# Performance work log

Measured on AMD Instinct MI355X. Metric: run time of the kernel, lower is better.

## Reference

```python
import jax, jax.numpy as jnp
import numpy as np

HIDDEN = 512
BATCH = 32
SEQ = 4096


def setup_inputs() -> dict:
    key = jax.random.key(0)
    ks = jax.random.split(key, 8)
    s = 1.0 / np.sqrt(HIDDEN)
    return {
        "encoder_outputs": jax.random.normal(ks[0], (BATCH, SEQ, HIDDEN), jnp.float32),
        "decoder_hidden": jax.random.normal(ks[1], (BATCH, HIDDEN), jnp.float32),
        "W_enc": jax.random.uniform(ks[2], (HIDDEN, HIDDEN), jnp.float32, -s, s),
        "b_enc": jax.random.uniform(ks[3], (HIDDEN,), jnp.float32, -s, s),
        "W_dec": jax.random.uniform(ks[4], (HIDDEN, HIDDEN), jnp.float32, -s, s),
        "b_dec": jax.random.uniform(ks[5], (HIDDEN,), jnp.float32, -s, s),
        "W_v": jax.random.uniform(ks[6], (HIDDEN, 1), jnp.float32, -s, s),
        "b_v": jax.random.uniform(ks[7], (1,), jnp.float32, -s, s),
    }


def reference(encoder_outputs, decoder_hidden, W_enc, b_enc, W_dec, b_dec, W_v, b_v):
    # (b, s, h) projected encoder states
    enc_proj = jnp.einsum("bsh,hk->bsk", encoder_outputs, W_enc) + b_enc
    # (b, 1, h) projected decoder state, broadcast-added over seq
    dec_proj = (decoder_hidden @ W_dec + b_dec)[:, None, :]
    # score: (b, s, 1)
    score = jnp.tanh(enc_proj + dec_proj) @ W_v + b_v
    attention_weights = jax.nn.softmax(score, axis=1)  # softmax over seq_len
    # context: (b, h) weighted sum of encoder outputs
    context = jnp.sum(attention_weights * encoder_outputs, axis=1)
    return context, jnp.squeeze(attention_weights, -1)
```

## Files before the change

### kernel.cpp

```cpp
#include <hip/hip_runtime.h>
#include <hip/hip_bf16.h>

typedef __attribute__((ext_vector_type(8))) short bf16x8;
typedef __attribute__((ext_vector_type(4))) float f32x4;

#define HID 512
#define NB 32
#define SEQL 4096
#define BM 64
#define NBLK 2048

#define WS_BP    0
#define WS_DPROJ (512*1024)
#define WS_SUM   (576*1024)

__device__ __forceinline__ short f2bf(float f) {
    unsigned u = __float_as_uint(f);
    unsigned r = (u + 0x7fffu + ((u >> 16) & 1u)) >> 16;
    return (short)r;
}

__device__ __forceinline__ float fast_tanh(float x) {
    float e = __expf(2.0f * x);
    float r = __builtin_amdgcn_rcpf(e + 1.0f);
    return 1.0f - 2.0f * r;
}

__device__ __forceinline__ void async16(const void* g, void* l) {
    __builtin_amdgcn_global_load_lds((__attribute__((address_space(1))) void*)(g),
                                     (__attribute__((address_space(3))) void*)(l),
                                     16, 0, 0);
}

__global__ void k_pre(const float* __restrict__ We, short* __restrict__ Bp,
                      const float* __restrict__ dec, const float* __restrict__ Wd,
                      const float* __restrict__ be, const float* __restrict__ bd,
                      float* __restrict__ dproj, float* __restrict__ out,
                      float* __restrict__ sumacc) {
    const int blk = blockIdx.x, t = threadIdx.x;
    if (blk < 128) {
        int tid  = blk * 256 + t;
        int lane = tid & 63;
        int nt   = (tid >> 6) & 31;
        int kc   = tid >> 11;
        int k0   = kc * 32 + (lane >> 4) * 8;
        int n    = nt * 16 + (lane & 15);
        bf16x8 v;
#pragma unroll
        for (int j = 0; j < 8; ++j) v[j] = f2bf(We[(size_t)(k0 + j) * HID + n]);
        *(bf16x8*)&Bp[(size_t)tid * 8] = v;
    } else if (blk < 640) {
        __shared__ float red[8][33];
        int bid2 = blk - 128;
        int b  = bid2 >> 4, kg = bid2 & 15;
        int kl = t & 31,    hc = t >> 5;
        int k  = kg * 32 + kl;
        const float* dr = dec + (size_t)b * HID;
        float a = 0.f;
#pragma unroll 8
        for (int j = 0; j < 64; ++j) {
            int h = hc * 64 + j;
            a += dr[h] * Wd[(size_t)h * HID + k];
        }
        red[hc][kl] = a;
        __syncthreads();
        if (hc == 0) {
            float s = be[k] + bd[k];
#pragma unroll
            for (int c = 0; c < 8; ++c) s += red[c][kl];
            dproj[(size_t)b * HID + k] = s;
        }
    } else {
        int bz = blk - 640;
        out[bz * 256 + t] = 0.f;
        if (bz == 0 && t < NB) sumacc[t] = 0.f;
    }
}

__global__ __launch_bounds__(256, 2)
void k_main(const float* __restrict__ E, const short* __restrict__ Bp,
            const float* __restrict__ dproj, const float* __restrict__ Wv,
            float* __restrict__ out, float* __restrict__ sumacc) {
    __shared__ short As[2][BM][40];
    __shared__ short Bs[2][32 * HID];
    __shared__ float fbuf[640];
    __shared__ float pbuf[BM];

    const int tid  = threadIdx.x;
    const int wave = tid >> 6, lane = tid & 63;
    const int quad = lane >> 4, l15 = lane & 15;
    const int bid  = blockIdx.x;
    const int row0 = bid * BM;
    const int b    = bid >> 6;

    f32x4 acc[4][8];
#pragma unroll
    for (int r = 0; r < 4; ++r)
#pragma unroll
        for (int c = 0; c < 8; ++c) acc[r][c] = (f32x4){0.f, 0.f, 0.f, 0.f};

    const int arow = tid >> 2, ac8 = (tid & 3) * 8;
    const float* aptr = E + (size_t)(row0 + arow) * HID + ac8;

    {
        float4 a0 = *(const float4*)(aptr);
        float4 a1 = *(const float4*)(aptr + 4);
#pragma unroll
        for (int i = 0; i < 8; ++i) {
            int off = (i * 4 + wave) * 512;
            async16(Bp + off + lane * 8, &Bs[0][off]);
        }
        bf16x8 av;
        av[0] = f2bf(a0.x); av[1] = f2bf(a0.y); av[2] = f2bf(a0.z); av[3] = f2bf(a0.w);
        av[4] = f2bf(a1.x); av[5] = f2bf(a1.y); av[6] = f2bf(a1.z); av[7] = f2bf(a1.w);
        *(bf16x8*)&As[0][arow][ac8] = av;
        __syncthreads();
    }

    for (int kc = 0; kc < 16; ++kc) {
        const int cur = kc & 1, nxt = cur ^ 1;
        float4 a0, a1;
        if (kc < 15) {
            a0 = *(const float4*)(aptr + (kc + 1) * 32);
            a1 = *(const float4*)(aptr + (kc + 1) * 32 + 4);
            const short* bsrc = Bp + (size_t)(kc + 1) * 16384;
#pragma unroll
            for (int i = 0; i < 8; ++i) {
                int off = (i * 4 + wave) * 512;
                async16(bsrc + off + lane * 8, &Bs[nxt][off]);
            }
        }
        bf16x8 fa[4];
#pragma unroll
        for (int r = 0; r < 4; ++r)
            fa[r] = *(bf16x8*)&As[cur][r * 16 + l15][quad * 8];
#pragma unroll
        for (int c = 0; c < 8; ++c) {
            int nt = wave * 8 + c;
            bf16x8 fb = *(bf16x8*)&Bs[cur][(nt * 64 + lane) * 8];
#pragma unroll
            for (int r = 0; r < 4; ++r)
                acc[r][c] = __builtin_amdgcn_mfma_f32_16x16x32_bf16(fa[r], fb, acc[r][c], 0, 0, 0);
        }
        if (kc < 15) {
            bf16x8 av;
            av[0] = f2bf(a0.x); av[1] = f2bf(a0.y); av[2] = f2bf(a0.z); av[3] = f2bf(a0.w);
            av[4] = f2bf(a1.x); av[5] = f2bf(a1.y); av[6] = f2bf(a1.z); av[7] = f2bf(a1.w);
            *(bf16x8*)&As[nxt][arow][ac8] = av;
        }
        __syncthreads();
    }

    float part[4][4];
#pragma unroll
    for (int r = 0; r < 4; ++r)
#pragma unroll
        for (int g = 0; g < 4; ++g) part[r][g] = 0.f;
    const float* dp = dproj + (size_t)b * HID;
#pragma unroll
    for (int c = 0; c < 8; ++c) {
        int col = wave * 128 + c * 16 + l15;
        float dv = dp[col];
        float wv = Wv[col];
#pragma unroll
        for (int r = 0; r < 4; ++r)
#pragma unroll
            for (int g = 0; g < 4; ++g)
                part[r][g] += fast_tanh(acc[r][c][g] + dv) * wv;
    }
#pragma unroll
    for (int r = 0; r < 4; ++r)
#pragma unroll
        for (int g = 0; g < 4; ++g) {
            float v = part[r][g];
            v += __shfl_xor(v, 1); v += __shfl_xor(v, 2);
            v += __shfl_xor(v, 4); v += __shfl_xor(v, 8);
            part[r][g] = v;
        }
    if (l15 == 0) {
#pragma unroll
        for (int r = 0; r < 4; ++r)
#pragma unroll
            for (int g = 0; g < 4; ++g)
                fbuf[wave * 64 + r * 16 + quad * 4 + g] = part[r][g];
    }
    __syncthreads();
    if (tid < 64) {
        float s  = fbuf[tid] + fbuf[64 + tid] + fbuf[128 + tid] + fbuf[192 + tid];
        float pv = __expf(s);
        pbuf[tid] = pv;
        out[(size_t)NB * HID + row0 + tid] = pv;
        float t2 = pv;
        t2 += __shfl_xor(t2, 1);  t2 += __shfl_xor(t2, 2);  t2 += __shfl_xor(t2, 4);
        t2 += __shfl_xor(t2, 8);  t2 += __shfl_xor(t2, 16); t2 += __shfl_xor(t2, 32);
        if (tid == 0) atomicAdd(&sumacc[b], t2);
    }
    __syncthreads();

    const int hq = tid & 127, rh = tid >> 7;
    const float4* E4 = (const float4*)E;
    size_t cbase = (size_t)(row0 + rh * 32) * (HID / 4) + hq;
    float4 ca = {0.f, 0.f, 0.f, 0.f};
#pragma unroll 4
    for (int rr = 0; rr < 32; ++rr) {
        float w  = pbuf[rh * 32 + rr];
        float4 e = E4[cbase + (size_t)rr * (HID / 4)];
        ca.x += w * e.x; ca.y += w * e.y; ca.z += w * e.z; ca.w += w * e.w;
    }
    if (rh == 1) {
        fbuf[hq] = ca.x; fbuf[128 + hq] = ca.y; fbuf[256 + hq] = ca.z; fbuf[384 + hq] = ca.w;
    }
    __syncthreads();
    if (rh == 0) {
        ca.x += fbuf[hq]; ca.y += fbuf[128 + hq]; ca.z += fbuf[256 + hq]; ca.w += fbuf[384 + hq];
        float* cg = out + (size_t)b * HID + hq * 4;
        atomicAdd(cg + 0, ca.x); atomicAdd(cg + 1, ca.y);
        atomicAdd(cg + 2, ca.z); atomicAdd(cg + 3, ca.w);
    }
}

__global__ void k_finish(float* __restrict__ out, const float* __restrict__ sumacc) {
    int idx = blockIdx.x * 256 + threadIdx.x;
    if (idx < NB * HID) {
        out[idx] *= 1.0f / sumacc[idx >> 9];
    } else {
        int w = idx - NB * HID;
        out[idx] *= 1.0f / sumacc[w >> 12];
    }
}

extern "C" void kernel_launch(void* const* d_in, const int* in_sizes, int n_in,
                              void* d_out, int out_size, void* d_ws, size_t ws_size,
                              hipStream_t stream) {
    const float* E   = (const float*)d_in[0];
    const float* dec = (const float*)d_in[1];
    const float* We  = (const float*)d_in[2];
    const float* be  = (const float*)d_in[3];
    const float* Wd  = (const float*)d_in[4];
    const float* bd  = (const float*)d_in[5];
    const float* Wv  = (const float*)d_in[6];
    float* out = (float*)d_out;
    char*  ws  = (char*)d_ws;
    short* Bp     = (short*)(ws + WS_BP);
    float* dproj  = (float*)(ws + WS_DPROJ);
    float* sumacc = (float*)(ws + WS_SUM);

    k_pre<<<704, 256, 0, stream>>>(We, Bp, dec, Wd, be, bd, dproj, out, sumacc);
    k_main<<<NBLK, 256, 0, stream>>>(E, Bp, dproj, Wv, out, sumacc);
    k_finish<<<576, 256, 0, stream>>>(out, sumacc);
}
```

Baseline: 458.4 us.

## Load A fragments directly into registers, stagger K start, use packed bf16 convert

Drops the LDS staging buffer for the encoder tile. Each wave now loads its own MFMA A fragments straight from global memory into registers and converts them with the hardware packed bf16 conversion instruction. The start of the K loop is rotated per block so concurrent blocks read different slices of the packed weight matrix, and the loop uses a hand-placed waitcnt, barrier and sched_barrier structure to overlap the next loads with the MFMAs. This removes the LDS writes, the LDS reads and one barrier for A per K step. In exchange, each of the four waves reads the same A data, so global and L1 traffic for A rises about fourfold.

New measurement: 519.8 us. 1.13x slower.

```diff
diff --git a/kernel.cpp b/kernel.cpp
--- a/kernel.cpp
+++ b/kernel.cpp
@@ -24,6 +24,18 @@
     float e = __expf(2.0f * x);
     float r = __builtin_amdgcn_rcpf(e + 1.0f);
     return 1.0f - 2.0f * r;
+}
+
+__device__ __forceinline__ unsigned cvtpk(float lo, float hi) {
+    unsigned r;
+    asm("v_cvt_pk_bf16_f32 %0, %1, %2" : "=v"(r) : "v"(lo), "v"(hi));
+    return r;
+}
+__device__ __forceinline__ bf16x8 pack8(const float4& A, const float4& B) {
+    union { unsigned u[4]; bf16x8 v; } t;
+    t.u[0] = cvtpk(A.x, A.y); t.u[1] = cvtpk(A.z, A.w);
+    t.u[2] = cvtpk(B.x, B.y); t.u[3] = cvtpk(B.z, B.w);
+    return t.v;
 }
 
 __device__ __forceinline__ void async16(const void* g, void* l) {
@@ -81,7 +93,6 @@
 void k_main(const float* __restrict__ E, const short* __restrict__ Bp,
             const float* __restrict__ dproj, const float* __restrict__ Wv,
             float* __restrict__ out, float* __restrict__ sumacc) {
-    __shared__ short As[2][BM][40];
     __shared__ short Bs[2][32 * HID];
     __shared__ float fbuf[640];
     __shared__ float pbuf[BM];
@@ -92,6 +103,7 @@
     const int bid  = blockIdx.x;
     const int row0 = bid * BM;
     const int b    = bid >> 6;
+    const int stag = bid & 15;
 
     f32x4 acc[4][8];
 #pragma unroll
@@ -99,56 +111,66 @@
 #pragma unroll
         for (int c = 0; c < 8; ++c) acc[r][c] = (f32x4){0.f, 0.f, 0.f, 0.f};
 
-    const int arow = tid >> 2, ac8 = (tid & 3) * 8;
-    const float* aptr = E + (size_t)(row0 + arow) * HID + ac8;
-
+    const float* aE = E + (size_t)(row0 + l15) * HID + quad * 8;
+
+    int kcs = stag;
     {
-        float4 a0 = *(const float4*)(aptr);
-        float4 a1 = *(const float4*)(aptr + 4);
+        const short* bsrc = Bp + (size_t)kcs * 16384;
 #pragma unroll
         for (int i = 0; i < 8; ++i) {
             int off = (i * 4 + wave) * 512;
-            async16(Bp + off + lane * 8, &Bs[0][off]);
-        }
-        bf16x8 av;
-        av[0] = f2bf(a0.x); av[1] = f2bf(a0.y); av[2] = f2bf(a0.z); av[3] = f2bf(a0.w);
-        av[4] = f2bf(a1.x); av[5] = f2bf(a1.y); av[6] = f2bf(a1.z); av[7] = f2bf(a1.w);
-        *(bf16x8*)&As[0][arow][ac8] = av;
-        __syncthreads();
-    }
+            async16(bsrc + off + lane * 8, &Bs[0][off]);
+        }
+    }
+    __builtin_amdgcn_sched_barrier(0);
+    float4 c0a = *(const float4*)(aE + 0 * 8192 + kcs * 32);
+    float4 c0b = *(const float4*)(aE + 0 * 8192 + kcs * 32 + 4);
+    float4 c1a = *(const float4*)(aE + 1 * 8192 + kcs * 32);
+    float4 c1b = *(const float4*)(aE + 1 * 8192 + kcs * 32 + 4);
+    float4 c2a = *(const float4*)(aE + 2 * 8192 + kcs * 32);
+    float4 c2b = *(const float4*)(aE + 2 * 8192 + kcs * 32 + 4);
+    float4 c3a = *(const float4*)(aE + 3 * 8192 + kcs * 32);
+    float4 c3b = *(const float4*)(aE + 3 * 8192 + kcs * 32 + 4);
+    __builtin_amdgcn_sched_barrier(0);
 
     for (int kc = 0; kc < 16; ++kc) {
         const int cur = kc & 1, nxt = cur ^ 1;
-        float4 a0, a1;
+        asm volatile("s_waitcnt vmcnt(8)" ::: "memory");
+        __builtin_amdgcn_s_barrier();
+        __builtin_amdgcn_sched_barrier(0);
+        bf16x8 fa[4];
+        fa[0] = pack8(c0a, c0b); fa[1] = pack8(c1a, c1b);
+        fa[2] = pack8(c2a, c2b); fa[3] = pack8(c3a, c3b);
+        __builtin_amdgcn_sched_barrier(0);
+        const int kn = (kcs + 1) & 15;
         if (kc < 15) {
-            a0 = *(const float4*)(aptr + (kc + 1) * 32);
-            a1 = *(const float4*)(aptr + (kc + 1) * 32 + 4);
-            const short* bsrc = Bp + (size_t)(kc + 1) * 16384;
+            const short* bsrc = Bp + (size_t)kn * 16384;
 #pragma unroll
             for (int i = 0; i < 8; ++i) {
                 int off = (i * 4 + wave) * 512;
                 async16(bsrc + off + lane * 8, &Bs[nxt][off]);
             }
         }
-        bf16x8 fa[4];
-#pragma unroll
-        for (int r = 0; r < 4; ++r)
-            fa[r] = *(bf16x8*)&As[cur][r * 16 + l15][quad * 8];
+        __builtin_amdgcn_sched_barrier(0);
+        if (kc < 15) {
+            c0a = *(const float4*)(aE + 0 * 8192 + kn * 32);
+            c0b = *(const float4*)(aE + 0 * 8192 + kn * 32 + 4);
+            c1a = *(const float4*)(aE + 1 * 8192 + kn * 32);
+            c1b = *(const float4*)(aE + 1 * 8192 + kn * 32 + 4);
+            c2a = *(const float4*)(aE + 2 * 8192 + kn * 32);
+            c2b = *(const float4*)(aE + 2 * 8192 + kn * 32 + 4);
+            c3a = *(const float4*)(aE + 3 * 8192 + kn * 32);
+            c3b = *(const float4*)(aE + 3 * 8192 + kn * 32 + 4);
+        }
+        __builtin_amdgcn_sched_barrier(0);
 #pragma unroll
         for (int c = 0; c < 8; ++c) {
-            int nt = wave * 8 + c;
-            bf16x8 fb = *(bf16x8*)&Bs[cur][(nt * 64 + lane) * 8];
+            bf16x8 fb = *(bf16x8*)&Bs[cur][(wave * 8 + c) * 512 + lane * 8];
 #pragma unroll
             for (int r = 0; r < 4; ++r)
                 acc[r][c] = __builtin_amdgcn_mfma_f32_16x16x32_bf16(fa[r], fb, acc[r][c], 0, 0, 0);
         }
-        if (kc < 15) {
-            bf16x8 av;
-            av[0] = f2bf(a0.x); av[1] = f2bf(a0.y); av[2] = f2bf(a0.z); av[3] = f2bf(a0.w);
-            av[4] = f2bf(a1.x); av[5] = f2bf(a1.y); av[6] = f2bf(a1.z); av[7] = f2bf(a1.w);
-            *(bf16x8*)&As[nxt][arow][ac8] = av;
-        }
-        __syncthreads();
+        kcs = kn;
     }
 
     float part[4][4];
```
